# Kernel tuning notes

Measured on AMD Instinct MI355X. Metric: run time of the kernel, lower is better.

The kernel has to match this reference:

```python
import jax, jax.numpy as jnp
import numpy as np

B, C, H, W = 8, 256, 64, 64


def setup_inputs() -> dict:
    key = jax.random.key(0)
    ks = jax.random.split(key, 8)
    s = 1.0 / np.sqrt(C)
    return {
        "x": jax.random.normal(ks[0], (B, C, H, W), dtype=jnp.float32),
        "Wq": jax.random.normal(ks[1], (C, C), dtype=jnp.float32) * s,
        "bq": jax.random.normal(ks[2], (C,), dtype=jnp.float32) * 0.01,
        "Wk": jax.random.normal(ks[3], (C, C), dtype=jnp.float32) * s,
        "bk": jax.random.normal(ks[4], (C,), dtype=jnp.float32) * 0.01,
        "Wv": jax.random.normal(ks[5], (C, C), dtype=jnp.float32) * s,
        "bv": jax.random.normal(ks[6], (C,), dtype=jnp.float32) * 0.01,
        "gamma": jax.random.normal(ks[7], (1,), dtype=jnp.float32) * 0.1,
    }


def reference(x, Wq, bq, Wk, bk, Wv, bv, gamma):
    b, c, h, w = x.shape
    xf = x.reshape(b, c, h * w)                       # (B, C, N)
    # 1x1 conv == per-pixel linear: out_c = W @ in_c + bias
    q = jnp.einsum('oc,bcn->bon', Wq, xf) + bq[None, :, None]
    k = jnp.einsum('oc,bcn->bon', Wk, xf) + bk[None, :, None]
    v = jnp.einsum('oc,bcn->bon', Wv, xf) + bv[None, :, None]
    # attention_map[b, i, j] = sum_c q[b, c, i] * k[b, c, j]  (no scaling in original)
    scores = jnp.einsum('bci,bcj->bij', q, k)         # (B, N, N)
    attn = jax.nn.softmax(scores, axis=-1)
    # out[b, c, i] = sum_j v[b, c, j] * attn[b, i, j]
    out = jnp.einsum('bcj,bij->bci', v, attn)
    out = out.reshape(b, c, h, w)
    return x + gamma[0] * out
```

## Files before the change

kernel.cpp:

```cpp
#include <hip/hip_runtime.h>

#define BATCH 8
#define CCH 256
#define NPOS 4096

typedef __bf16 bf16x8 __attribute__((ext_vector_type(8)));
typedef float f32x4 __attribute__((ext_vector_type(4)));
typedef int i32x4 __attribute__((ext_vector_type(4)));

typedef const __attribute__((address_space(1))) void GAS;
typedef __attribute__((address_space(3))) void LAS;

#define CFENCE() __asm__ volatile("" ::: "memory")
#define WAIT_VM8()  do { CFENCE(); __builtin_amdgcn_s_waitcnt(0x0F78); CFENCE(); } while (0)
#define WAIT_LGKM0() do { CFENCE(); __builtin_amdgcn_s_waitcnt(0xC07F); CFENCE(); } while (0)
#define BAR_RAW() do { CFENCE(); __builtin_amdgcn_s_barrier(); CFENCE(); } while (0)

__device__ __forceinline__ unsigned short f2bf(float f) {
  unsigned u = __builtin_bit_cast(unsigned, f);
  u += 0x7fffu + ((u >> 16) & 1u);
  return (unsigned short)(u >> 16);
}

__device__ __forceinline__ bf16x8 ld_bf8(const unsigned short* p) {
  i32x4 t = *reinterpret_cast<const i32x4*>(p);
  return __builtin_bit_cast(bf16x8, t);
}

__global__ void cvt_kernel(const float* __restrict__ Wq,
                           const float* __restrict__ Wk,
                           const float* __restrict__ Wv,
                           unsigned short* __restrict__ dst)
{
  const int idx = blockIdx.x * 256 + threadIdx.x;
  const float* src = (idx < 65536) ? Wq : ((idx < 131072) ? Wk : Wv);
  dst[idx] = f2bf(src[idx & 65535]);
}

__global__ __launch_bounds__(256, 3)
void qkv_kernel(const float* __restrict__ x,
                const unsigned short* __restrict__ Wall,
                const float* __restrict__ bq,
                const float* __restrict__ bk,
                const float* __restrict__ bv,
                unsigned short* __restrict__ qT,
                unsigned short* __restrict__ kT,
                unsigned short* __restrict__ vG)
{
  __shared__ __align__(16) unsigned short xT[64 * 264];
  __shared__ __align__(16) unsigned short tbuf[64 * 72];

  const int b     = blockIdx.x;
  const int i0    = blockIdx.y * 64;
  const int obase = blockIdx.z * 64;
  const int tid = threadIdx.x;
  const int w   = tid >> 6;
  const int l   = tid & 63;
  const int n   = l & 15;
  const int q4  = l >> 4;

  {
    const float* xp = x + ((size_t)b * CCH + tid) * NPOS + i0;
#pragma unroll
    for (int it = 0; it < 16; ++it) {
      f32x4 f = *reinterpret_cast<const f32x4*>(xp + it * 4);
#pragma unroll
      for (int e = 0; e < 4; ++e) xT[(it * 4 + e) * 264 + tid] = f2bf(f[e]);
    }
  }
  __syncthreads();

  const size_t qbase = (size_t)b * NPOS * CCH;

  for (int s = 0; s < 3; ++s) {
    const unsigned short* Wp = Wall + s * 65536 + (size_t)(obase + w * 16 + n) * CCH + q4 * 8;
    bf16x8 wfr[8];
#pragma unroll
    for (int kk = 0; kk < 8; ++kk) wfr[kk] = ld_bf8(Wp + kk * 32);

    const float* bias = (s == 0) ? bq : (s == 1) ? bk : bv;
    float bo[4];
#pragma unroll
    for (int r = 0; r < 4; ++r) bo[r] = bias[obase + w * 16 + q4 * 4 + r];

    f32x4 acc[4];
#pragma unroll
    for (int pt = 0; pt < 4; ++pt) {
      acc[pt] = {0.f, 0.f, 0.f, 0.f};
#pragma unroll
      for (int kk = 0; kk < 8; ++kk) {
        bf16x8 bfr = ld_bf8(&xT[(pt * 16 + n) * 264 + kk * 32 + q4 * 8]);
        acc[pt] = __builtin_amdgcn_mfma_f32_16x16x32_bf16(wfr[kk], bfr, acc[pt], 0, 0, 0);
      }
    }

    if (s) __syncthreads();
    if (s < 2) {
#pragma unroll
      for (int pt = 0; pt < 4; ++pt)
#pragma unroll
        for (int r = 0; r < 4; ++r)
          tbuf[(pt * 16 + n) * 72 + w * 16 + q4 * 4 + r] = f2bf(acc[pt][r] + bo[r]);
    } else {
#pragma unroll
      for (int pt = 0; pt < 4; ++pt)
#pragma unroll
        for (int r = 0; r < 4; ++r)
          tbuf[(w * 16 + q4 * 4 + r) * 72 + pt * 16 + n] = f2bf(acc[pt][r] + bo[r]);
    }
    __syncthreads();

    if (s < 2) {
      unsigned short* dst = (s == 0 ? qT : kT) + qbase;
#pragma unroll
      for (int it = 0; it < 2; ++it) {
        const int idx = it * 256 + tid;
        const int pos = idx >> 3, ow = (idx & 7) * 8;
        i32x4 d = *reinterpret_cast<const i32x4*>(&tbuf[pos * 72 + ow]);
        *reinterpret_cast<i32x4*>(&dst[(size_t)(i0 + pos) * CCH + obase + ow]) = d;
      }
    } else {
#pragma unroll
      for (int it = 0; it < 2; ++it) {
        const int idx = it * 256 + tid;
        const int o = idx >> 3, pw = (idx & 7) * 8;
        i32x4 d = *reinterpret_cast<const i32x4*>(&tbuf[o * 72 + pw]);
        *reinterpret_cast<i32x4*>(&vG[qbase + (size_t)(obase + o) * NPOS + i0 + pw]) = d;
      }
    }
  }
}

__global__ __launch_bounds__(256, 2)
void attn_kernel(const unsigned short* __restrict__ qT,
                 const unsigned short* __restrict__ kT,
                 const unsigned short* __restrict__ vG,
                 const float* __restrict__ x,
                 const float* __restrict__ gamma,
                 float* __restrict__ out)
{
  __shared__ __align__(16) unsigned short kbuf[2][64 * 256];
  __shared__ __align__(16) unsigned short pbuf[64 * 72];
  __shared__ float stat_lds[64];

  const int b   = blockIdx.x;
  const int i0  = blockIdx.y * 64;
  const int tid = threadIdx.x;
  const int w   = tid >> 6;
  const int l   = tid & 63;
  const int n   = l & 15;
  const int q4  = l >> 4;
  const int nsw = n & 7;

  const unsigned short* qTb = qT + (size_t)b * NPOS * CCH;
  const unsigned short* kTb = kT + (size_t)b * NPOS * CCH;
  const unsigned short* vb  = vG + (size_t)b * NPOS * CCH;

  bf16x8 afr[8];
  {
    const unsigned short* qrow = qTb + (size_t)(i0 + w * 16 + n) * CCH + q4 * 8;
#pragma unroll
    for (int kk = 0; kk < 8; ++kk)
      afr[kk] = ld_bf8(qrow + kk * 32);
  }

  {
#pragma unroll
    for (int it = 0; it < 8; ++it) {
      const int t = w * 8 + it;
      const int j = 2 * t + (l >> 5);
      const int gp = l & 31;
      const int g  = gp ^ (j & 7);
      const unsigned short* src = kTb + (size_t)j * CCH + g * 8;
      unsigned short* dst = &kbuf[0][t * 512];
      __builtin_amdgcn_global_load_lds((GAS*)src, (LAS*)dst, 16, 0, 0);
    }
  }

  f32x4 O[16];
#pragma unroll
  for (int t = 0; t < 16; ++t) O[t] = {0.f, 0.f, 0.f, 0.f};
  float mrow[4] = {-1e30f, -1e30f, -1e30f, -1e30f};
  float lrow[4] = {0.f, 0.f, 0.f, 0.f};

  for (int jt = 0; jt < 64; ++jt) {
    const int j0 = jt * 64;
    const unsigned short* kb = kbuf[jt & 1];

    i32x4 vreg[8];
#pragma unroll
    for (int ct = 0; ct < 4; ++ct) {
      const unsigned short* vp = vb + (size_t)(w * 64 + ct * 16 + n) * NPOS + j0 + q4 * 8;
      vreg[ct * 2]     = *reinterpret_cast<const i32x4*>(vp);
      vreg[ct * 2 + 1] = *reinterpret_cast<const i32x4*>(vp + 32);
    }

    WAIT_VM8();
    BAR_RAW();

    f32x4 sacc[4];
#pragma unroll
    for (int nt = 0; nt < 4; ++nt) {
      const unsigned short* krow = kb + (nt * 16 + n) * 256;
      sacc[nt] = {0.f, 0.f, 0.f, 0.f};
#pragma unroll
      for (int kk = 0; kk < 8; ++kk) {
        const int gp = (kk * 4 + q4) ^ nsw;
        bf16x8 bfr = ld_bf8(krow + gp * 8);
        sacc[nt] = __builtin_amdgcn_mfma_f32_16x16x32_bf16(afr[kk], bfr, sacc[nt], 0, 0, 0);
      }
    }

    float a_r[4];
#pragma unroll
    for (int r = 0; r < 4; ++r) {
      float tm = fmaxf(fmaxf(sacc[0][r], sacc[1][r]), fmaxf(sacc[2][r], sacc[3][r]));
      tm = fmaxf(tm, __shfl_xor(tm, 1));
      tm = fmaxf(tm, __shfl_xor(tm, 2));
      tm = fmaxf(tm, __shfl_xor(tm, 4));
      tm = fmaxf(tm, __shfl_xor(tm, 8));
      const float mnew = fmaxf(mrow[r], tm);
      a_r[r] = __expf(mrow[r] - mnew);
      float s = 0.f;
#pragma unroll
      for (int nt = 0; nt < 4; ++nt) {
        const float p = __expf(sacc[nt][r] - mnew);
        sacc[nt][r] = p;
        s += p;
      }
      s += __shfl_xor(s, 1);
      s += __shfl_xor(s, 2);
      s += __shfl_xor(s, 4);
      s += __shfl_xor(s, 8);
      lrow[r] = lrow[r] * a_r[r] + s;
      mrow[r] = mnew;
    }

    if (n == 0) {
#pragma unroll
      for (int r = 0; r < 4; ++r) stat_lds[w * 16 + q4 * 4 + r] = a_r[r];
    }
#pragma unroll
    for (int r = 0; r < 4; ++r) {
      const int row = w * 16 + q4 * 4 + r;
#pragma unroll
      for (int nt = 0; nt < 4; ++nt)
        pbuf[row * 72 + nt * 16 + n] = f2bf(sacc[nt][r]);
    }

    {
      const int j0n = ((jt + 1) & 63) * 64;
      unsigned short* bufn = kbuf[(jt + 1) & 1];
#pragma unroll
      for (int it = 0; it < 8; ++it) {
        const int t = w * 8 + it;
        const int j = 2 * t + (l >> 5);
        const int gp = l & 31;
        const int g  = gp ^ (j & 7);
        const unsigned short* src = kTb + (size_t)(j0n + j) * CCH + g * 8;
        unsigned short* dst = &bufn[t * 512];
        __builtin_amdgcn_global_load_lds((GAS*)src, (LAS*)dst, 16, 0, 0);
      }
    }

    WAIT_LGKM0();
    BAR_RAW();

#pragma unroll
    for (int it = 0; it < 4; ++it) {
      const float al = stat_lds[it * 16 + n];
#pragma unroll
      for (int ct = 0; ct < 4; ++ct) {
        f32x4& o = O[ct * 4 + it];
        o[0] *= al; o[1] *= al; o[2] *= al; o[3] *= al;
      }
    }

    bf16x8 pf[8];
#pragma unroll
    for (int it = 0; it < 4; ++it) {
      pf[it * 2 + 0] = ld_bf8(&pbuf[(it * 16 + n) * 72 + q4 * 8]);
      pf[it * 2 + 1] = ld_bf8(&pbuf[(it * 16 + n) * 72 + 32 + q4 * 8]);
    }
#pragma unroll
    for (int ct = 0; ct < 4; ++ct) {
      bf16x8 vf0 = __builtin_bit_cast(bf16x8, vreg[ct * 2]);
      bf16x8 vf1 = __builtin_bit_cast(bf16x8, vreg[ct * 2 + 1]);
#pragma unroll
      for (int it = 0; it < 4; ++it) {
        O[ct * 4 + it] = __builtin_amdgcn_mfma_f32_16x16x32_bf16(vf0, pf[it * 2 + 0], O[ct * 4 + it], 0, 0, 0);
        O[ct * 4 + it] = __builtin_amdgcn_mfma_f32_16x16x32_bf16(vf1, pf[it * 2 + 1], O[ct * 4 + it], 0, 0, 0);
      }
    }
  }

  __syncthreads();
  if (n == 0) {
#pragma unroll
    for (int r = 0; r < 4; ++r) stat_lds[w * 16 + q4 * 4 + r] = lrow[r];
  }
  __syncthreads();

  const float g = gamma[0];
#pragma unroll
  for (int it = 0; it < 4; ++it) {
    const float sc = g / stat_lds[it * 16 + n];
    const int ipos = i0 + it * 16 + n;
#pragma unroll
    for (int ct = 0; ct < 4; ++ct) {
#pragma unroll
      for (int r = 0; r < 4; ++r) {
        const int c = w * 64 + ct * 16 + q4 * 4 + r;
        const size_t idx = ((size_t)(b * CCH + c)) * NPOS + ipos;
        out[idx] = x[idx] + sc * O[ct * 4 + it][r];
      }
    }
  }
}

extern "C" void kernel_launch(void* const* d_in, const int* in_sizes, int n_in,
                              void* d_out, int out_size, void* d_ws, size_t ws_size,
                              hipStream_t stream)
{
  const float* x     = (const float*)d_in[0];
  const float* Wq    = (const float*)d_in[1];
  const float* bq    = (const float*)d_in[2];
  const float* Wk    = (const float*)d_in[3];
  const float* bk    = (const float*)d_in[4];
  const float* Wv    = (const float*)d_in[5];
  const float* bv    = (const float*)d_in[6];
  const float* gamma = (const float*)d_in[7];
  float* out = (float*)d_out;

  unsigned short* ws   = (unsigned short*)d_ws;
  unsigned short* Wall = ws;
  unsigned short* qT   = ws + 196608;
  unsigned short* kT   = qT + (size_t)BATCH * NPOS * CCH;
  unsigned short* vG   = kT + (size_t)BATCH * NPOS * CCH;

  cvt_kernel<<<768, 256, 0, stream>>>(Wq, Wk, Wv, Wall);
  qkv_kernel<<<dim3(8, 64, 4), 256, 0, stream>>>(x, Wall, bq, bk, bv, qT, kT, vG);
  attn_kernel<<<dim3(8, 64), 256, 0, stream>>>(qT, kT, vG, x, gamma, out);
}
```

Measured before the change: 354.0 us.

## Split attention over key halves with merge kernel, exp2 softmax, direct K loads

Splits the key dimension into two halves so the attention grid doubles. Partial bf16 outputs plus per-row max and sum are written to workspace and combined by a new merge kernel, with a fallback when the workspace is too small. Also folds log2(e) into Wq and bq so the kernel can use exp2, and computes the row sum with an MFMA against a ones vector. K is now read straight from global into registers instead of being staged in LDS, and the QKV kernel loops over all output channel blocks in one block. The price is extra workspace traffic, an extra launch, and bf16 rounding of the partial outputs.

After: 1.165 ms. 3.29x slower.

```diff
diff --git a/kernel.cpp b/kernel.cpp
--- a/kernel.cpp
+++ b/kernel.cpp
@@ -3,16 +3,14 @@
 #define BATCH 8
 #define CCH 256
 #define NPOS 4096
+#define LOG2E 1.4426950408889634f
 
 typedef __bf16 bf16x8 __attribute__((ext_vector_type(8)));
 typedef float f32x4 __attribute__((ext_vector_type(4)));
 typedef int i32x4 __attribute__((ext_vector_type(4)));
-
-typedef const __attribute__((address_space(1))) void GAS;
-typedef __attribute__((address_space(3))) void LAS;
+typedef unsigned short us4 __attribute__((ext_vector_type(4)));
 
 #define CFENCE() __asm__ volatile("" ::: "memory")
-#define WAIT_VM8()  do { CFENCE(); __builtin_amdgcn_s_waitcnt(0x0F78); CFENCE(); } while (0)
 #define WAIT_LGKM0() do { CFENCE(); __builtin_amdgcn_s_waitcnt(0xC07F); CFENCE(); } while (0)
 #define BAR_RAW() do { CFENCE(); __builtin_amdgcn_s_barrier(); CFENCE(); } while (0)
 
@@ -21,7 +19,9 @@
   u += 0x7fffu + ((u >> 16) & 1u);
   return (unsigned short)(u >> 16);
 }
-
+__device__ __forceinline__ float bf2f(unsigned short s) {
+  return __builtin_bit_cast(float, ((unsigned)s) << 16);
+}
 __device__ __forceinline__ bf16x8 ld_bf8(const unsigned short* p) {
   i32x4 t = *reinterpret_cast<const i32x4*>(p);
   return __builtin_bit_cast(bf16x8, t);
@@ -34,7 +34,9 @@
 {
   const int idx = blockIdx.x * 256 + threadIdx.x;
   const float* src = (idx < 65536) ? Wq : ((idx < 131072) ? Wk : Wv);
-  dst[idx] = f2bf(src[idx & 65535]);
+  float v = src[idx & 65535];
+  if (idx < 65536) v *= LOG2E;
+  dst[idx] = f2bf(v);
 }
 
 __global__ __launch_bounds__(256, 3)
@@ -50,99 +52,6 @@
   __shared__ __align__(16) unsigned short xT[64 * 264];
   __shared__ __align__(16) unsigned short tbuf[64 * 72];
 
-  const int b     = blockIdx.x;
-  const int i0    = blockIdx.y * 64;
-  const int obase = blockIdx.z * 64;
-  const int tid = threadIdx.x;
-  const int w   = tid >> 6;
-  const int l   = tid & 63;
-  const int n   = l & 15;
-  const int q4  = l >> 4;
-
-  {
-    const float* xp = x + ((size_t)b * CCH + tid) * NPOS + i0;
-#pragma unroll
-    for (int it = 0; it < 16; ++it) {
-      f32x4 f = *reinterpret_cast<const f32x4*>(xp + it * 4);
-#pragma unroll
-      for (int e = 0; e < 4; ++e) xT[(it * 4 + e) * 264 + tid] = f2bf(f[e]);
-    }
-  }
-  __syncthreads();
-
-  const size_t qbase = (size_t)b * NPOS * CCH;
-
-  for (int s = 0; s < 3; ++s) {
-    const unsigned short* Wp = Wall + s * 65536 + (size_t)(obase + w * 16 + n) * CCH + q4 * 8;
-    bf16x8 wfr[8];
-#pragma unroll
-    for (int kk = 0; kk < 8; ++kk) wfr[kk] = ld_bf8(Wp + kk * 32);
-
-    const float* bias = (s == 0) ? bq : (s == 1) ? bk : bv;
-    float bo[4];
-#pragma unroll
-    for (int r = 0; r < 4; ++r) bo[r] = bias[obase + w * 16 + q4 * 4 + r];
-
-    f32x4 acc[4];
-#pragma unroll
-    for (int pt = 0; pt < 4; ++pt) {
-      acc[pt] = {0.f, 0.f, 0.f, 0.f};
-#pragma unroll
-      for (int kk = 0; kk < 8; ++kk) {
-        bf16x8 bfr = ld_bf8(&xT[(pt * 16 + n) * 264 + kk * 32 + q4 * 8]);
-        acc[pt] = __builtin_amdgcn_mfma_f32_16x16x32_bf16(wfr[kk], bfr, acc[pt], 0, 0, 0);
-      }
-    }
-
-    if (s) __syncthreads();
-    if (s < 2) {
-#pragma unroll
-      for (int pt = 0; pt < 4; ++pt)
-#pragma unroll
-        for (int r = 0; r < 4; ++r)
-          tbuf[(pt * 16 + n) * 72 + w * 16 + q4 * 4 + r] = f2bf(acc[pt][r] + bo[r]);
-    } else {
-#pragma unroll
-      for (int pt = 0; pt < 4; ++pt)
-#pragma unroll
-        for (int r = 0; r < 4; ++r)
-          tbuf[(w * 16 + q4 * 4 + r) * 72 + pt * 16 + n] = f2bf(acc[pt][r] + bo[r]);
-    }
-    __syncthreads();
-
-    if (s < 2) {
-      unsigned short* dst = (s == 0 ? qT : kT) + qbase;
-#pragma unroll
-      for (int it = 0; it < 2; ++it) {
-        const int idx = it * 256 + tid;
-        const int pos = idx >> 3, ow = (idx & 7) * 8;
-        i32x4 d = *reinterpret_cast<const i32x4*>(&tbuf[pos * 72 + ow]);
-        *reinterpret_cast<i32x4*>(&dst[(size_t)(i0 + pos) * CCH + obase + ow]) = d;
-      }
-    } else {
-#pragma unroll
-      for (int it = 0; it < 2; ++it) {
-        const int idx = it * 256 + tid;
-        const int o = idx >> 3, pw = (idx & 7) * 8;
-        i32x4 d = *reinterpret_cast<const i32x4*>(&tbuf[o * 72 + pw]);
-        *reinterpret_cast<i32x4*>(&vG[qbase + (size_t)(obase + o) * NPOS + i0 + pw]) = d;
-      }
-    }
-  }
-}
-
-__global__ __launch_bounds__(256, 2)
-void attn_kernel(const unsigned short* __restrict__ qT,
-                 const unsigned short* __restrict__ kT,
-                 const unsigned short* __restrict__ vG,
-                 const float* __restrict__ x,
-                 const float* __restrict__ gamma,
-                 float* __restrict__ out)
-{
-  __shared__ __align__(16) unsigned short kbuf[2][64 * 256];
-  __shared__ __align__(16) unsigned short pbuf[64 * 72];
-  __shared__ float stat_lds[64];
-
   const int b   = blockIdx.x;
   const int i0  = blockIdx.y * 64;
   const int tid = threadIdx.x;
@@ -150,6 +59,96 @@
   const int l   = tid & 63;
   const int n   = l & 15;
   const int q4  = l >> 4;
+
+  {
+    const float* xp = x + ((size_t)b * CCH + tid) * NPOS + i0;
+#pragma unroll
+    for (int it = 0; it < 16; ++it) {
+      f32x4 f = *reinterpret_cast<const f32x4*>(xp + it * 4);
+#pragma unroll
+      for (int e = 0; e < 4; ++e) xT[(it * 4 + e) * 264 + tid] = f2bf(f[e]);
+    }
+  }
+  __syncthreads();
+
+  const size_t qbase = (size_t)b * NPOS * CCH;
+
+  for (int z = 0; z < 4; ++z) {
+    const int obase = z * 64;
+    for (int s = 0; s < 3; ++s) {
+      const unsigned short* Wp = Wall + s * 65536 + (size_t)(obase + w * 16 + n) * CCH + q4 * 8;
+      bf16x8 wfr[8];
+#pragma unroll
+      for (int kk = 0; kk < 8; ++kk) wfr[kk] = ld_bf8(Wp + kk * 32);
+
+      const float* bias = (s == 0) ? bq : (s == 1) ? bk : bv;
+      const float bscale = (s == 0) ? LOG2E : 1.0f;
+      float bo[4];
+#pragma unroll
+      for (int r = 0; r < 4; ++r) bo[r] = bias[obase + w * 16 + q4 * 4 + r] * bscale;
+
+      f32x4 acc[4];
+#pragma unroll
+      for (int pt = 0; pt < 4; ++pt) {
+        acc[pt] = {0.f, 0.f, 0.f, 0.f};
+#pragma unroll
+        for (int kk = 0; kk < 8; ++kk) {
+          bf16x8 bfr = ld_bf8(&xT[(pt * 16 + n) * 264 + kk * 32 + q4 * 8]);
+          acc[pt] = __builtin_amdgcn_mfma_f32_16x16x32_bf16(wfr[kk], bfr, acc[pt], 0, 0, 0);
+        }
+      }
+
+      if (s < 2) {
+        unsigned short* dst = (s == 0 ? qT : kT) + qbase;
+#pragma unroll
+        for (int pt = 0; pt < 4; ++pt) {
+          us4 pk = { f2bf(acc[pt][0] + bo[0]), f2bf(acc[pt][1] + bo[1]),
+                     f2bf(acc[pt][2] + bo[2]), f2bf(acc[pt][3] + bo[3]) };
+          *reinterpret_cast<us4*>(&dst[(size_t)(i0 + pt * 16 + n) * CCH + obase + w * 16 + q4 * 4]) = pk;
+        }
+      } else {
+        __syncthreads();
+#pragma unroll
+        for (int pt = 0; pt < 4; ++pt)
+#pragma unroll
+          for (int r = 0; r < 4; ++r)
+            tbuf[(w * 16 + q4 * 4 + r) * 72 + pt * 16 + n] = f2bf(acc[pt][r] + bo[r]);
+        __syncthreads();
+#pragma unroll
+        for (int it = 0; it < 2; ++it) {
+          const int idx = it * 256 + tid;
+          const int o = idx >> 3, pw = (idx & 7) * 8;
+          i32x4 d = *reinterpret_cast<const i32x4*>(&tbuf[o * 72 + pw]);
+          *reinterpret_cast<i32x4*>(&vG[qbase + (size_t)(obase + o) * NPOS + i0 + pw]) = d;
+        }
+      }
+    }
+  }
+}
+
+template <int NZ>
+__global__ __launch_bounds__(256, 3)
+void attn_kernel(const unsigned short* __restrict__ qT,
+                 const unsigned short* __restrict__ kT,
+                 const unsigned short* __restrict__ vG,
+                 const float* __restrict__ x,
+                 const float* __restrict__ gamma,
+                 float* __restrict__ out,
+                 unsigned short* __restrict__ po,
+                 float* __restrict__ ml)
+{
+  __shared__ __align__(16) unsigned short pbuf[64 * 64];
+  __shared__ float stat_lds[64];
+
+  const int b   = blockIdx.x;
+  const int iy  = blockIdx.y;
+  const int i0  = iy * 64;
+  const int z   = (NZ == 2) ? blockIdx.z : 0;
+  const int tid = threadIdx.x;
+  const int w   = tid >> 6;
+  const int l   = tid & 63;
+  const int n   = l & 15;
+  const int q4  = l >> 4;
   const int nsw = n & 7;
 
   const unsigned short* qTb = qT + (size_t)b * NPOS * CCH;
@@ -163,29 +162,45 @@
     for (int kk = 0; kk < 8; ++kk)
       afr[kk] = ld_bf8(qrow + kk * 32);
   }
-
+  bf16x8 ones;
   {
-#pragma unroll
-    for (int it = 0; it < 8; ++it) {
-      const int t = w * 8 + it;
-      const int j = 2 * t + (l >> 5);
-      const int gp = l & 31;
-      const int g  = gp ^ (j & 7);
-      const unsigned short* src = kTb + (size_t)j * CCH + g * 8;
-      unsigned short* dst = &kbuf[0][t * 512];
-      __builtin_amdgcn_global_load_lds((GAS*)src, (LAS*)dst, 16, 0, 0);
-    }
+    i32x4 t = { (int)0x3F803F80, (int)0x3F803F80, (int)0x3F803F80, (int)0x3F803F80 };
+    ones = __builtin_bit_cast(bf16x8, t);
   }
 
   f32x4 O[16];
 #pragma unroll
   for (int t = 0; t < 16; ++t) O[t] = {0.f, 0.f, 0.f, 0.f};
+  f32x4 lacc = {0.f, 0.f, 0.f, 0.f};
   float mrow[4] = {-1e30f, -1e30f, -1e30f, -1e30f};
-  float lrow[4] = {0.f, 0.f, 0.f, 0.f};
-
-  for (int jt = 0; jt < 64; ++jt) {
-    const int j0 = jt * 64;
-    const unsigned short* kb = kbuf[jt & 1];
+
+  const int JT = 64 / NZ;
+  for (int jt = 0; jt < JT; ++jt) {
+    const int j0 = z * (NPOS / NZ) + jt * 64;
+
+    const unsigned short* rowptr = kTb + (size_t)j0 * CCH + n * CCH + q4 * 8;
+    i32x4 ka[4], kb2[4];
+#pragma unroll
+    for (int kk = 0; kk < 4; ++kk) ka[kk] = *reinterpret_cast<const i32x4*>(rowptr + kk * 32);
+    f32x4 sacc[4];
+#pragma unroll
+    for (int nt = 0; nt < 4; ++nt) {
+      const unsigned short* rp = rowptr + nt * 16 * CCH;
+#pragma unroll
+      for (int kk = 0; kk < 4; ++kk) kb2[kk] = *reinterpret_cast<const i32x4*>(rp + (kk + 4) * 32);
+      sacc[nt] = {0.f, 0.f, 0.f, 0.f};
+#pragma unroll
+      for (int kk = 0; kk < 4; ++kk)
+        sacc[nt] = __builtin_amdgcn_mfma_f32_16x16x32_bf16(afr[kk], __builtin_bit_cast(bf16x8, ka[kk]), sacc[nt], 0, 0, 0);
+      if (nt < 3) {
+        const unsigned short* rn = rowptr + (nt + 1) * 16 * CCH;
+#pragma unroll
+        for (int kk = 0; kk < 4; ++kk) ka[kk] = *reinterpret_cast<const i32x4*>(rn + kk * 32);
+      }
+#pragma unroll
+      for (int kk = 0; kk < 4; ++kk)
+        sacc[nt] = __builtin_amdgcn_mfma_f32_16x16x32_bf16(afr[kk + 4], __builtin_bit_cast(bf16x8, kb2[kk]), sacc[nt], 0, 0, 0);
+    }
 
     i32x4 vreg[8];
 #pragma unroll
@@ -193,22 +208,6 @@
       const unsigned short* vp = vb + (size_t)(w * 64 + ct * 16 + n) * NPOS + j0 + q4 * 8;
       vreg[ct * 2]     = *reinterpret_cast<const i32x4*>(vp);
       vreg[ct * 2 + 1] = *reinterpret_cast<const i32x4*>(vp + 32);
-    }
-
-    WAIT_VM8();
-    BAR_RAW();
-
-    f32x4 sacc[4];
-#pragma unroll
-    for (int nt = 0; nt < 4; ++nt) {
-      const unsigned short* krow = kb + (nt * 16 + n) * 256;
-      sacc[nt] = {0.f, 0.f, 0.f, 0.f};
-#pragma unroll
-      for (int kk = 0; kk < 8; ++kk) {
-        const int gp = (kk * 4 + q4) ^ nsw;
-        bf16x8 bfr = ld_bf8(krow + gp * 8);
-        sacc[nt] = __builtin_amdgcn_mfma_f32_16x16x32_bf16(afr[kk], bfr, sacc[nt], 0, 0, 0);
-      }
     }
 
     float a_r[4];
@@ -220,19 +219,10 @@
       tm = fmaxf(tm, __shfl_xor(tm, 4));
       tm = fmaxf(tm, __shfl_xor(tm, 8));
       const float mnew = fmaxf(mrow[r], tm);
-      a_r[r] = __expf(mrow[r] - mnew);
-      float s = 0.f;
-#pragma unroll
-      for (int nt = 0; nt < 4; ++nt) {
-        const float p = __expf(sacc[nt][r] - mnew);
-        sacc[nt][r] = p;
-        s += p;
-      }
-      s += __shfl_xor(s, 1);
-      s += __shfl_xor(s, 2);
-      s += __shfl_xor(s, 4);
-      s += __shfl_xor(s, 8);
-      lrow[r] = lrow[r] * a_r[r] + s;
+      a_r[r] = __builtin_amdgcn_exp2f(mrow[r] - mnew);
+#pragma unroll
+      for (int nt = 0; nt < 4; ++nt)
+        sacc[nt][r] = __builtin_amdgcn_exp2f(sacc[nt][r] - mnew);
       mrow[r] = mnew;
     }
 
@@ -243,45 +233,42 @@
 #pragma unroll
     for (int r = 0; r < 4; ++r) {
       const int row = w * 16 + q4 * 4 + r;
-#pragma unroll
-      for (int nt = 0; nt < 4; ++nt)
-        pbuf[row * 72 + nt * 16 + n] = f2bf(sacc[nt][r]);
-    }
-
-    {
-      const int j0n = ((jt + 1) & 63) * 64;
-      unsigned short* bufn = kbuf[(jt + 1) & 1];
-#pragma unroll
-      for (int it = 0; it < 8; ++it) {
-        const int t = w * 8 + it;
-        const int j = 2 * t + (l >> 5);
-        const int gp = l & 31;
-        const int g  = gp ^ (j & 7);
-        const unsigned short* src = kTb + (size_t)(j0n + j) * CCH + g * 8;
-        unsigned short* dst = &bufn[t * 512];
-        __builtin_amdgcn_global_load_lds((GAS*)src, (LAS*)dst, 16, 0, 0);
+      const int r7 = row & 7;
+#pragma unroll
+      for (int nt = 0; nt < 4; ++nt) {
+        const int chunk = nt * 2 + (n >> 3);
+        pbuf[row * 64 + (chunk ^ r7) * 8 + nsw] = f2bf(sacc[nt][r]);
       }
     }
 
     WAIT_LGKM0();
     BAR_RAW();
 
+    float al[4];
+#pragma unroll
+    for (int it = 0; it < 4; ++it) al[it] = stat_lds[it * 16 + n];
+
+    bf16x8 pf[8];
 #pragma unroll
     for (int it = 0; it < 4; ++it) {
-      const float al = stat_lds[it * 16 + n];
+      const int rw = it * 16 + n;
+      const int r7 = rw & 7;
+      pf[it * 2 + 0] = ld_bf8(&pbuf[rw * 64 + ((q4) ^ r7) * 8]);
+      pf[it * 2 + 1] = ld_bf8(&pbuf[rw * 64 + ((4 + q4) ^ r7) * 8]);
+    }
+
+#pragma unroll
+    for (int it = 0; it < 4; ++it) {
 #pragma unroll
       for (int ct = 0; ct < 4; ++ct) {
         f32x4& o = O[ct * 4 + it];
-        o[0] *= al; o[1] *= al; o[2] *= al; o[3] *= al;
-      }
-    }
-
-    bf16x8 pf[8];
-#pragma unroll
-    for (int it = 0; it < 4; ++it) {
-      pf[it * 2 + 0] = ld_bf8(&pbuf[(it * 16 + n) * 72 + q4 * 8]);
-      pf[it * 2 + 1] = ld_bf8(&pbuf[(it * 16 + n) * 72 + 32 + q4 * 8]);
-    }
+        o[0] *= al[it]; o[1] *= al[it]; o[2] *= al[it]; o[3] *= al[it];
+      }
+    }
+    lacc[0] *= al[w]; lacc[1] *= al[w]; lacc[2] *= al[w]; lacc[3] *= al[w];
+    lacc = __builtin_amdgcn_mfma_f32_16x16x32_bf16(ones, pf[w * 2 + 0], lacc, 0, 0, 0);
+    lacc = __builtin_amdgcn_mfma_f32_16x16x32_bf16(ones, pf[w * 2 + 1], lacc, 0, 0, 0);
+
 #pragma unroll
     for (int ct = 0; ct < 4; ++ct) {
       bf16x8 vf0 = __builtin_bit_cast(bf16x8, vreg[ct * 2]);
@@ -292,29 +279,95 @@
         O[ct * 4 + it] = __builtin_amdgcn_mfma_f32_16x16x32_bf16(vf1, pf[it * 2 + 1], O[ct * 4 + it], 0, 0, 0);
       }
     }
-  }
-
+
+    BAR_RAW();
+  }
+
+  if (NZ == 2) {
+    const int part = ((b * 64 + iy) * 2 + z);
+    unsigned short* poB = po + (size_t)part * (64 * 256);
+#pragma unroll
+    for (int it = 0; it < 4; ++it) {
+#pragma unroll
+      for (int ct = 0; ct < 4; ++ct) {
+        f32x4 o = O[ct * 4 + it];
+        us4 pk = { f2bf(o[0]), f2bf(o[1]), f2bf(o[2]), f2bf(o[3]) };
+        *reinterpret_cast<us4*>(&poB[(it * 16 + n) * 256 + w * 64 + ct * 16 + q4 * 4]) = pk;
+      }
+    }
+    float* mlB = ml + (size_t)part * 128;
+    if (n == 0) {
+#pragma unroll
+      for (int r = 0; r < 4; ++r) mlB[w * 16 + q4 * 4 + r] = mrow[r];
+    }
+    if (q4 == 0) mlB[64 + w * 16 + n] = lacc[0];
+  } else {
+    __syncthreads();
+    if (q4 == 0) stat_lds[w * 16 + n] = lacc[0];
+    __syncthreads();
+    const float g = gamma[0];
+#pragma unroll
+    for (int it = 0; it < 4; ++it) {
+      const float sc = g / stat_lds[it * 16 + n];
+      const int ipos = i0 + it * 16 + n;
+#pragma unroll
+      for (int ct = 0; ct < 4; ++ct) {
+#pragma unroll
+        for (int r = 0; r < 4; ++r) {
+          const int c = w * 64 + ct * 16 + q4 * 4 + r;
+          const size_t idx = ((size_t)(b * CCH + c)) * NPOS + ipos;
+          out[idx] = x[idx] + sc * O[ct * 4 + it][r];
+        }
+      }
+    }
+  }
+}
+
+__global__ __launch_bounds__(256, 2)
+void merge_kernel(const unsigned short* __restrict__ po,
+                  const float* __restrict__ ml,
+                  const float* __restrict__ x,
+                  const float* __restrict__ gamma,
+                  float* __restrict__ out)
+{
+  __shared__ float num[64 * 257];
+  __shared__ float a1s[64], a2s[64], dns[64];
+
+  const int b  = blockIdx.x;
+  const int iy = blockIdx.y;
+  const int i0 = iy * 64;
+  const int tid = threadIdx.x;
+  const int p0 = (b * 64 + iy) * 2;
+
+  if (tid < 64) {
+    const float m1 = ml[(size_t)p0 * 128 + tid];
+    const float l1 = ml[(size_t)p0 * 128 + 64 + tid];
+    const float m2 = ml[(size_t)(p0 + 1) * 128 + tid];
+    const float l2 = ml[(size_t)(p0 + 1) * 128 + 64 + tid];
+    const float m = fmaxf(m1, m2);
+    const float a1 = __builtin_amdgcn_exp2f(m1 - m);
+    const float a2 = __builtin_amdgcn_exp2f(m2 - m);
+    a1s[tid] = a1;
+    a2s[tid] = a2;
+    dns[tid] = gamma[0] / (l1 * a1 + l2 * a2);
+  }
   __syncthreads();
-  if (n == 0) {
-#pragma unroll
-    for (int r = 0; r < 4; ++r) stat_lds[w * 16 + q4 * 4 + r] = lrow[r];
+
+  const unsigned short* po1 = po + (size_t)p0 * (64 * 256);
+  const unsigned short* po2 = po1 + 64 * 256;
+  for (int i = 0; i < 64; ++i) {
+    num[i * 257 + tid] = bf2f(po1[i * 256 + tid]) * a1s[i] + bf2f(po2[i * 256 + tid]) * a2s[i];
   }
   __syncthreads();
 
-  const float g = gamma[0];
-#pragma unroll
-  for (int it = 0; it < 4; ++it) {
-    const float sc = g / stat_lds[it * 16 + n];
-    const int ipos = i0 + it * 16 + n;
-#pragma unroll
-    for (int ct = 0; ct < 4; ++ct) {
-#pragma unroll
-      for (int r = 0; r < 4; ++r) {
-        const int c = w * 64 + ct * 16 + q4 * 4 + r;
-        const size_t idx = ((size_t)(b * CCH + c)) * NPOS + ipos;
-        out[idx] = x[idx] + sc * O[ct * 4 + it][r];
-      }
-    }
+  const int il = tid & 63;
+  const int ch = tid >> 6;
+  const float dn = dns[il];
+#pragma unroll 4
+  for (int k = 0; k < 64; ++k) {
+    const int c = ch * 64 + k;
+    const size_t idx = ((size_t)(b * CCH + c)) * NPOS + i0 + il;
+    out[idx] = x[idx] + dn * num[il * 257 + c];
   }
 }
 
@@ -337,8 +390,17 @@
   unsigned short* qT   = ws + 196608;
   unsigned short* kT   = qT + (size_t)BATCH * NPOS * CCH;
   unsigned short* vG   = kT + (size_t)BATCH * NPOS * CCH;
+  unsigned short* po   = vG + (size_t)BATCH * NPOS * CCH;
+  float*          ml   = (float*)(po + (size_t)1024 * 64 * 256);
+
+  const size_t need_split = (size_t)((char*)(ml + 1024 * 128) - (char*)d_ws);
 
   cvt_kernel<<<768, 256, 0, stream>>>(Wq, Wk, Wv, Wall);
-  qkv_kernel<<<dim3(8, 64, 4), 256, 0, stream>>>(x, Wall, bq, bk, bv, qT, kT, vG);
-  attn_kernel<<<dim3(8, 64), 256, 0, stream>>>(qT, kT, vG, x, gamma, out);
-}
+  qkv_kernel<<<dim3(8, 64), 256, 0, stream>>>(x, Wall, bq, bk, bv, qT, kT, vG);
+  if (ws_size >= need_split) {
+    attn_kernel<2><<<dim3(8, 64, 2), 256, 0, stream>>>(qT, kT, vG, x, gamma, out, po, ml);
+    merge_kernel<<<dim3(8, 64), 256, 0, stream>>>(po, ml, x, gamma, out);
+  } else {
+    attn_kernel<1><<<dim3(8, 64), 256, 0, stream>>>(qT, kT, vG, x, gamma, out, po, ml);
+  }
+}
```
